# Optimization experiments

Measured on AMD Instinct MI355X. Metric: run time of the kernel, lower is better.

The kernel has to match this reference:

```python
import jax, jax.numpy as jnp
import numpy as np

B, S, C, MID = 32, 8192, 256, 128

def setup_inputs() -> dict:
    key = jax.random.key(0)
    k_x, k_w1, k_b1, k_w2, k_b2 = jax.random.split(key, 5)
    bound1 = 1.0 / np.sqrt(C)
    bound2 = 1.0 / np.sqrt(MID)
    return {
        "x": jax.random.normal(k_x, (B, S, C), dtype=jnp.float32),
        "W1": jax.random.uniform(k_w1, (C, MID), jnp.float32, -bound1, bound1),
        "b1": jax.random.uniform(k_b1, (MID,), jnp.float32, -bound1, bound1),
        "w2": jax.random.uniform(k_w2, (MID,), jnp.float32, -bound2, bound2),
        "b2": jax.random.uniform(k_b2, (), jnp.float32, -bound2, bound2),
    }

def reference(x, W1, b1, w2, b2):
    # scores: (B, S) — dropout is identity in eval mode
    h = jnp.tanh(jnp.einsum("bsc,cm->bsm", x, W1) + b1)       # (B, S, MID)
    scores = jnp.einsum("bsm,m->bs", h, w2) + b2              # (B, S)
    attn = jax.nn.softmax(scores, axis=-1)                    # softmax over seq
    out = jnp.einsum("bsc,bs->bc", x, attn)                   # weighted sum over seq
    return out
```

## Files before the change

### kernel.cpp

```cpp
#include <hip/hip_runtime.h>
#include <hip/hip_bf16.h>


typedef __attribute__((ext_vector_type(8))) short short8;
typedef __attribute__((ext_vector_type(4))) float f32x4;
typedef unsigned short u16;

constexpr int Bb = 32;
constexpr int Ss = 8192;
constexpr int Cc = 256;
constexpr int MIDm = 128;
constexpr int BM = 128;
constexpr int BK = 64;
constexpr int NCH = Cc / BK;
constexpr int NBLK = Bb * Ss / BM;
constexpr int BPB = Ss / BM;

__device__ __forceinline__ u16 f2bf(float f) {
  return __builtin_bit_cast(u16, __float2bfloat16(f));
}

__global__ __launch_bounds__(256) void wprep_kernel(
    const float* __restrict__ W1, u16* __restrict__ FB)
{
  const int t    = blockIdx.x * 256 + threadIdx.x;
  const int lane = t & 63;
  const int nt   = (t >> 6) & 3;
  const int kg   = (t >> 8) & 1;
  const int kc   = (t >> 9) & 3;
  const int wc   = (t >> 11) & 1;
  const int n    = wc * 64 + nt * 16 + (lane & 15);
  const int k0   = kc * 64 + kg * 32 + (lane >> 4) * 8;
  union { u16 v[8]; short8 s; } u;
  #pragma unroll
  for (int e = 0; e < 8; ++e) u.v[e] = f2bf(W1[(size_t)(k0 + e) * MIDm + n]);
  *(short8*)(FB + (size_t)t * 8) = u.s;
}

__global__ __launch_bounds__(256, 2) void fused_kernel(
    const float* __restrict__ x, const u16* __restrict__ FB,
    const float* __restrict__ b1, const float* __restrict__ w2,
    float* __restrict__ oPart, float* __restrict__ mPart, float* __restrict__ lPart)
{
  __shared__ __align__(16) float sX[2][BM * BK];
  __shared__ float sScore[2][BM];
  __shared__ float sP[BM];
  __shared__ float sMB, sLB;
  __shared__ __align__(16) float sO[4][Cc];

  const int tid  = threadIdx.x;
  const int lane = tid & 63;
  const int w    = tid >> 6;
  const int wr   = w >> 1;
  const int wc   = w & 1;
  const int q    = lane >> 4;
  const int ln   = lane & 15;
  const int row0 = blockIdx.x * BM;

  f32x4 acc[4][4];
  #pragma unroll
  for (int nt = 0; nt < 4; ++nt) {
    float bj = b1[64 * wc + 16 * nt + ln];
    #pragma unroll
    for (int mt = 0; mt < 4; ++mt) {
      acc[mt][nt][0] = bj; acc[mt][nt][1] = bj; acc[mt][nt][2] = bj; acc[mt][nt][3] = bj;
    }
  }

  const u16* fb = FB + ((size_t)wc * 2048 + lane) * 8;
  #define LDFRAG(kc, kg, nt) (*(const short8*)(fb + ((size_t)(kc)*512 + (kg)*256 + (nt)*64) * 8))

  #define STAGE(buf, kc)                                                              \
    {                                                                                 \
      _Pragma("unroll")                                                               \
      for (int r = 0; r < 8; ++r) {                                                   \
        int L    = r * 4096 + tid * 16;                                               \
        int row  = L >> 8;                                                            \
        int colb = (L & 255) ^ ((row & 7) << 4);                                      \
        const char* src = (const char*)x                                              \
            + ((size_t)(row0 + row) * Cc + (kc) * BK) * 4 + colb;                     \
        __builtin_amdgcn_global_load_lds(                                             \
            (const __attribute__((address_space(1))) void*)src,                       \
            (__attribute__((address_space(3))) void*)((char*)&sX[buf][0] + L),        \
            16, 0, 0);                                                                \
      }                                                                               \
    }

  short8 bfr[2][8];

  STAGE(0, 0);
  #pragma unroll
  for (int i = 0; i < 8; ++i) bfr[0][i] = LDFRAG(0, i >> 2, i & 3);
  __syncthreads();

  #pragma unroll
  for (int kc = 0; kc < NCH; ++kc) {
    const int cur = kc & 1;
    if (kc < NCH - 1) {
      STAGE(1 - cur, kc + 1);
      #pragma unroll
      for (int i = 0; i < 8; ++i) bfr[1 - cur][i] = LDFRAG(kc + 1, i >> 2, i & 3);
    }

    #pragma unroll
    for (int kg = 0; kg < 2; ++kg) {
      short8 af[4];
      #pragma unroll
      for (int mt = 0; mt < 4; ++mt) {
        const int row = 64 * wr + 16 * mt + ln;
        const int s   = (row & 7) << 4;
        const int c   = kg * 128 + q * 32;
        const char* base = (const char*)&sX[cur][0] + row * 256;
        float4 lo = *(const float4*)(base + ((c) ^ s));
        float4 hi = *(const float4*)(base + ((c + 16) ^ s));
        union { u16 v[8]; short8 s8; } t8;
        t8.v[0] = f2bf(lo.x); t8.v[1] = f2bf(lo.y); t8.v[2] = f2bf(lo.z); t8.v[3] = f2bf(lo.w);
        t8.v[4] = f2bf(hi.x); t8.v[5] = f2bf(hi.y); t8.v[6] = f2bf(hi.z); t8.v[7] = f2bf(hi.w);
        af[mt] = t8.s8;
      }
      #pragma unroll
      for (int nt = 0; nt < 4; ++nt)
        #pragma unroll
        for (int mt = 0; mt < 4; ++mt)
          acc[mt][nt] = __builtin_amdgcn_mfma_f32_16x16x32_bf16(
              af[mt], bfr[cur][kg * 4 + nt], acc[mt][nt], 0, 0, 0);
    }
    if (kc < NCH - 1) __syncthreads();
  }

  float w2v[4];
  #pragma unroll
  for (int nt = 0; nt < 4; ++nt) w2v[nt] = w2[64 * wc + 16 * nt + ln];

  float p[4][4];
  #pragma unroll
  for (int mt = 0; mt < 4; ++mt)
    #pragma unroll
    for (int r = 0; r < 4; ++r) p[mt][r] = 0.f;

  #pragma unroll
  for (int mt = 0; mt < 4; ++mt)
    #pragma unroll
    for (int nt = 0; nt < 4; ++nt)
      #pragma unroll
      for (int r = 0; r < 4; ++r)
        p[mt][r] += (1.0f - 2.0f / (__expf(2.0f * acc[mt][nt][r]) + 1.0f)) * w2v[nt];

  #pragma unroll
  for (int off = 1; off < 16; off <<= 1)
    #pragma unroll
    for (int mt = 0; mt < 4; ++mt)
      #pragma unroll
      for (int r = 0; r < 4; ++r)
        p[mt][r] += __shfl_xor(p[mt][r], off);

  __syncthreads();
  if (ln == 0) {
    #pragma unroll
    for (int mt = 0; mt < 4; ++mt)
      #pragma unroll
      for (int r = 0; r < 4; ++r)
        sScore[wc][64 * wr + 16 * mt + 4 * q + r] = p[mt][r];
  }
  __syncthreads();

  if (tid < BM) sP[tid] = sScore[0][tid] + sScore[1][tid];
  __syncthreads();
  if (w == 0) {
    float a = sP[lane], b = sP[lane + 64];
    float m = fmaxf(a, b);
    #pragma unroll
    for (int off = 1; off < 64; off <<= 1) m = fmaxf(m, __shfl_xor(m, off));
    float e0 = __expf(a - m), e1 = __expf(b - m);
    sP[lane] = e0; sP[lane + 64] = e1;
    float s = e0 + e1;
    #pragma unroll
    for (int off = 1; off < 64; off <<= 1) s += __shfl_xor(s, off);
    if (lane == 0) { sMB = m; sLB = s; }
  }
  __syncthreads();

  const int c4 = tid & 63;
  const int rg = tid >> 6;
  const float* xo = x + (size_t)(row0 + rg * 32) * Cc + c4 * 4;
  float4 o = make_float4(0.f, 0.f, 0.f, 0.f);
  #pragma unroll 8
  for (int r = 0; r < 32; ++r) {
    float pw = sP[rg * 32 + r];
    float4 xv = *(const float4*)(xo + (size_t)r * Cc);
    o.x = fmaf(pw, xv.x, o.x);
    o.y = fmaf(pw, xv.y, o.y);
    o.z = fmaf(pw, xv.z, o.z);
    o.w = fmaf(pw, xv.w, o.w);
  }
  *(float4*)&sO[rg][c4 * 4] = o;
  __syncthreads();

  float oc = sO[0][tid] + sO[1][tid] + sO[2][tid] + sO[3][tid];
  oPart[(size_t)blockIdx.x * Cc + tid] = oc;
  if (tid == 0) { mPart[blockIdx.x] = sMB; lPart[blockIdx.x] = sLB; }
}

__global__ __launch_bounds__(256) void combine_kernel(
    const float* __restrict__ oPart, const float* __restrict__ mPart,
    const float* __restrict__ lPart, float* __restrict__ out)
{
  const int b = blockIdx.x;
  const int t = threadIdx.x;
  float M = -3.4e38f;
  for (int k = 0; k < BPB; ++k) M = fmaxf(M, mPart[b * BPB + k]);
  float num = 0.f, den = 0.f;
  for (int k = 0; k < BPB; ++k) {
    float wgt = __expf(mPart[b * BPB + k] - M);
    den += wgt * lPart[b * BPB + k];
    num = fmaf(wgt, oPart[(size_t)(b * BPB + k) * Cc + t], num);
  }
  out[b * Cc + t] = num / den;
}

extern "C" void kernel_launch(void* const* d_in, const int* in_sizes, int n_in,
                              void* d_out, int out_size, void* d_ws, size_t ws_size,
                              hipStream_t stream)
{
  const float* x  = (const float*)d_in[0];
  const float* W1 = (const float*)d_in[1];
  const float* b1 = (const float*)d_in[2];
  const float* w2 = (const float*)d_in[3];
  float* out = (float*)d_out;

  u16*   FB    = (u16*)d_ws;
  float* oPart = (float*)((char*)d_ws + 65536);
  float* mPart = (float*)((char*)d_ws + 65536 + 2097152);
  float* lPart = (float*)((char*)d_ws + 65536 + 2097152 + 8192);

  wprep_kernel<<<16, 256, 0, stream>>>(W1, FB);
  fused_kernel<<<NBLK, 256, 0, stream>>>(x, FB, b1, w2, oPart, mPart, lPart);
  combine_kernel<<<Bb, Cc, 0, stream>>>(oPart, mPart, lPart, out);
}
```

Baseline: 97.35 us.

## Load x fragments directly from global into registers, drop LDS staging

Replaces the LDS double-buffered staging of x (global_load_lds with swizzle, plus block barriers) with per-thread direct global float4 loads into registers. These are prefetched two k-steps ahead, and the W1 fragment layout is re-indexed to 32-wide k chunks to match. This removes LDS traffic, the syncthreads per chunk and a big shared allocation, which may raise occupancy. In exchange, the two column-half waves both fetch the same x rows from global/L2, and register pressure goes up from holding the prefetched fragments.

```diff
diff --git a/kernel.cpp b/kernel.cpp
--- a/kernel.cpp
+++ b/kernel.cpp
@@ -11,8 +11,6 @@
 constexpr int Cc = 256;
 constexpr int MIDm = 128;
 constexpr int BM = 128;
-constexpr int BK = 64;
-constexpr int NCH = Cc / BK;
 constexpr int NBLK = Bb * Ss / BM;
 constexpr int BPB = Ss / BM;
 
@@ -26,11 +24,10 @@
   const int t    = blockIdx.x * 256 + threadIdx.x;
   const int lane = t & 63;
   const int nt   = (t >> 6) & 3;
-  const int kg   = (t >> 8) & 1;
-  const int kc   = (t >> 9) & 3;
+  const int kcc  = (t >> 8) & 7;
   const int wc   = (t >> 11) & 1;
   const int n    = wc * 64 + nt * 16 + (lane & 15);
-  const int k0   = kc * 64 + kg * 32 + (lane >> 4) * 8;
+  const int k0   = kcc * 32 + (lane >> 4) * 8;
   union { u16 v[8]; short8 s; } u;
   #pragma unroll
   for (int e = 0; e < 8; ++e) u.v[e] = f2bf(W1[(size_t)(k0 + e) * MIDm + n]);
@@ -42,7 +39,6 @@
     const float* __restrict__ b1, const float* __restrict__ w2,
     float* __restrict__ oPart, float* __restrict__ mPart, float* __restrict__ lPart)
 {
-  __shared__ __align__(16) float sX[2][BM * BK];
   __shared__ float sScore[2][BM];
   __shared__ float sP[BM];
   __shared__ float sMB, sLB;
@@ -57,6 +53,13 @@
   const int ln   = lane & 15;
   const int row0 = blockIdx.x * BM;
 
+  const float* pA[4];
+  #pragma unroll
+  for (int mt = 0; mt < 4; ++mt)
+    pA[mt] = x + (size_t)(row0 + 64 * wr + 16 * mt + ln) * Cc + q * 8;
+
+  const u16* fb = FB + ((size_t)wc * 2048 + lane) * 8;
+
   f32x4 acc[4][4];
   #pragma unroll
   for (int nt = 0; nt < 4; ++nt) {
@@ -67,65 +70,48 @@
     }
   }
 
-  const u16* fb = FB + ((size_t)wc * 2048 + lane) * 8;
-  #define LDFRAG(kc, kg, nt) (*(const short8*)(fb + ((size_t)(kc)*512 + (kg)*256 + (nt)*64) * 8))
-
-  #define STAGE(buf, kc)                                                              \
-    {                                                                                 \
-      _Pragma("unroll")                                                               \
-      for (int r = 0; r < 8; ++r) {                                                   \
-        int L    = r * 4096 + tid * 16;                                               \
-        int row  = L >> 8;                                                            \
-        int colb = (L & 255) ^ ((row & 7) << 4);                                      \
-        const char* src = (const char*)x                                              \
-            + ((size_t)(row0 + row) * Cc + (kc) * BK) * 4 + colb;                     \
-        __builtin_amdgcn_global_load_lds(                                             \
-            (const __attribute__((address_space(1))) void*)src,                       \
-            (__attribute__((address_space(3))) void*)((char*)&sX[buf][0] + L),        \
-            16, 0, 0);                                                                \
-      }                                                                               \
+  float4 A0[2][4], A1[2][4];
+  short8 Bf[2][4];
+
+  #define LOADA(ph, kk)                                                  \
+    { _Pragma("unroll")                                                  \
+      for (int mt = 0; mt < 4; ++mt) {                                   \
+        const float* p = pA[mt] + (kk) * 32;                             \
+        A0[ph][mt] = *(const float4*)p;                                  \
+        A1[ph][mt] = *(const float4*)(p + 4);                            \
+      } }
+  #define LOADB(ph, kk)                                                  \
+    { _Pragma("unroll")                                                  \
+      for (int nt = 0; nt < 4; ++nt)                                     \
+        Bf[ph][nt] = *(const short8*)(fb + ((size_t)(kk) * 256 + nt * 64) * 8); }
+
+  LOADA(0, 0) LOADB(0, 0)
+  LOADA(1, 1) LOADB(1, 1)
+
+  #pragma unroll
+  for (int kcc = 0; kcc < 8; ++kcc) {
+    const int ph = kcc & 1;
+
+    short8 af[4];
+    #pragma unroll
+    for (int mt = 0; mt < 4; ++mt) {
+      union { u16 v[8]; short8 s; } t8;
+      t8.v[0] = f2bf(A0[ph][mt].x); t8.v[1] = f2bf(A0[ph][mt].y);
+      t8.v[2] = f2bf(A0[ph][mt].z); t8.v[3] = f2bf(A0[ph][mt].w);
+      t8.v[4] = f2bf(A1[ph][mt].x); t8.v[5] = f2bf(A1[ph][mt].y);
+      t8.v[6] = f2bf(A1[ph][mt].z); t8.v[7] = f2bf(A1[ph][mt].w);
+      af[mt] = t8.s;
     }
-
-  short8 bfr[2][8];
-
-  STAGE(0, 0);
-  #pragma unroll
-  for (int i = 0; i < 8; ++i) bfr[0][i] = LDFRAG(0, i >> 2, i & 3);
-  __syncthreads();
-
-  #pragma unroll
-  for (int kc = 0; kc < NCH; ++kc) {
-    const int cur = kc & 1;
-    if (kc < NCH - 1) {
-      STAGE(1 - cur, kc + 1);
-      #pragma unroll
-      for (int i = 0; i < 8; ++i) bfr[1 - cur][i] = LDFRAG(kc + 1, i >> 2, i & 3);
-    }
-
-    #pragma unroll
-    for (int kg = 0; kg < 2; ++kg) {
-      short8 af[4];
-      #pragma unroll
-      for (int mt = 0; mt < 4; ++mt) {
-        const int row = 64 * wr + 16 * mt + ln;
-        const int s   = (row & 7) << 4;
-        const int c   = kg * 128 + q * 32;
-        const char* base = (const char*)&sX[cur][0] + row * 256;
-        float4 lo = *(const float4*)(base + ((c) ^ s));
-        float4 hi = *(const float4*)(base + ((c + 16) ^ s));
-        union { u16 v[8]; short8 s8; } t8;
-        t8.v[0] = f2bf(lo.x); t8.v[1] = f2bf(lo.y); t8.v[2] = f2bf(lo.z); t8.v[3] = f2bf(lo.w);
-        t8.v[4] = f2bf(hi.x); t8.v[5] = f2bf(hi.y); t8.v[6] = f2bf(hi.z); t8.v[7] = f2bf(hi.w);
-        af[mt] = t8.s8;
-      }
-      #pragma unroll
-      for (int nt = 0; nt < 4; ++nt)
-        #pragma unroll
-        for (int mt = 0; mt < 4; ++mt)
-          acc[mt][nt] = __builtin_amdgcn_mfma_f32_16x16x32_bf16(
-              af[mt], bfr[cur][kg * 4 + nt], acc[mt][nt], 0, 0, 0);
-    }
-    if (kc < NCH - 1) __syncthreads();
+    if (kcc < 6) LOADA(ph, kcc + 2)
+
+    #pragma unroll
+    for (int nt = 0; nt < 4; ++nt)
+      #pragma unroll
+      for (int mt = 0; mt < 4; ++mt)
+        acc[mt][nt] = __builtin_amdgcn_mfma_f32_16x16x32_bf16(
+            af[mt], Bf[ph][nt], acc[mt][nt], 0, 0, 0);
+
+    if (kcc < 6) LOADB(ph, kcc + 2)
   }
 
   float w2v[4];
@@ -154,7 +140,6 @@
       for (int r = 0; r < 4; ++r)
         p[mt][r] += __shfl_xor(p[mt][r], off);
 
-  __syncthreads();
   if (ln == 0) {
     #pragma unroll
     for (int mt = 0; mt < 4; ++mt)
```

Measured after the change: 129.0 us. 32.5% more time.

## Halve K-chunk to 32 and raise occupancy to four blocks per CU

Applied to the files above, without the earlier changes.

Reduces the staged x tile from 64 to 32 columns, so shared memory per block drops from about 64KB to about 32KB. The B-fragment register buffers are halved and launch bounds are raised to 4 blocks per CU to allow more resident waves to hide global-load latency. The weight-fragment layout in the prep kernel and the swizzled LDS staging are rewritten to match the 32-wide chunk. It also drops one barrier before the score write, and the chunk loop now has twice as many iterations and barriers.

```diff
diff --git a/kernel.cpp b/kernel.cpp
--- a/kernel.cpp
+++ b/kernel.cpp
@@ -11,7 +11,7 @@
 constexpr int Cc = 256;
 constexpr int MIDm = 128;
 constexpr int BM = 128;
-constexpr int BK = 64;
+constexpr int BK = 32;
 constexpr int NCH = Cc / BK;
 constexpr int NBLK = Bb * Ss / BM;
 constexpr int BPB = Ss / BM;
@@ -26,23 +26,22 @@
   const int t    = blockIdx.x * 256 + threadIdx.x;
   const int lane = t & 63;
   const int nt   = (t >> 6) & 3;
-  const int kg   = (t >> 8) & 1;
-  const int kc   = (t >> 9) & 3;
+  const int kcc  = (t >> 8) & 7;
   const int wc   = (t >> 11) & 1;
   const int n    = wc * 64 + nt * 16 + (lane & 15);
-  const int k0   = kc * 64 + kg * 32 + (lane >> 4) * 8;
+  const int k0   = kcc * 32 + (lane >> 4) * 8;
   union { u16 v[8]; short8 s; } u;
   #pragma unroll
   for (int e = 0; e < 8; ++e) u.v[e] = f2bf(W1[(size_t)(k0 + e) * MIDm + n]);
   *(short8*)(FB + (size_t)t * 8) = u.s;
 }
 
-__global__ __launch_bounds__(256, 2) void fused_kernel(
+__global__ __launch_bounds__(256, 4) void fused_kernel(
     const float* __restrict__ x, const u16* __restrict__ FB,
     const float* __restrict__ b1, const float* __restrict__ w2,
     float* __restrict__ oPart, float* __restrict__ mPart, float* __restrict__ lPart)
 {
-  __shared__ __align__(16) float sX[2][BM * BK];
+  __shared__ __align__(16) char sX[2][BM * BK * 4];
   __shared__ float sScore[2][BM];
   __shared__ float sP[BM];
   __shared__ float sMB, sLB;
@@ -68,29 +67,29 @@
   }
 
   const u16* fb = FB + ((size_t)wc * 2048 + lane) * 8;
-  #define LDFRAG(kc, kg, nt) (*(const short8*)(fb + ((size_t)(kc)*512 + (kg)*256 + (nt)*64) * 8))
+  #define LDFRAG(kcc, nt) (*(const short8*)(fb + ((size_t)(kcc) * 256 + (nt) * 64) * 8))
 
   #define STAGE(buf, kc)                                                              \
     {                                                                                 \
       _Pragma("unroll")                                                               \
-      for (int r = 0; r < 8; ++r) {                                                   \
-        int L    = r * 4096 + tid * 16;                                               \
-        int row  = L >> 8;                                                            \
-        int colb = (L & 255) ^ ((row & 7) << 4);                                      \
+      for (int r = 0; r < 4; ++r) {                                                   \
+        int L   = r * 4096 + tid * 16;                                                \
+        int row = L >> 7;                                                             \
+        int cb  = (L & 127) ^ ((row & 7) << 4);                                       \
         const char* src = (const char*)x                                              \
-            + ((size_t)(row0 + row) * Cc + (kc) * BK) * 4 + colb;                     \
+            + ((size_t)(row0 + row) * Cc + (size_t)(kc) * BK) * 4 + cb;               \
         __builtin_amdgcn_global_load_lds(                                             \
             (const __attribute__((address_space(1))) void*)src,                       \
-            (__attribute__((address_space(3))) void*)((char*)&sX[buf][0] + L),        \
+            (__attribute__((address_space(3))) void*)(&sX[buf][0] + L),               \
             16, 0, 0);                                                                \
       }                                                                               \
     }
 
-  short8 bfr[2][8];
+  short8 bfr[2][4];
 
   STAGE(0, 0);
   #pragma unroll
-  for (int i = 0; i < 8; ++i) bfr[0][i] = LDFRAG(0, i >> 2, i & 3);
+  for (int nt = 0; nt < 4; ++nt) bfr[0][nt] = LDFRAG(0, nt);
   __syncthreads();
 
   #pragma unroll
@@ -99,31 +98,23 @@
     if (kc < NCH - 1) {
       STAGE(1 - cur, kc + 1);
       #pragma unroll
-      for (int i = 0; i < 8; ++i) bfr[1 - cur][i] = LDFRAG(kc + 1, i >> 2, i & 3);
-    }
-
-    #pragma unroll
-    for (int kg = 0; kg < 2; ++kg) {
-      short8 af[4];
-      #pragma unroll
-      for (int mt = 0; mt < 4; ++mt) {
-        const int row = 64 * wr + 16 * mt + ln;
-        const int s   = (row & 7) << 4;
-        const int c   = kg * 128 + q * 32;
-        const char* base = (const char*)&sX[cur][0] + row * 256;
-        float4 lo = *(const float4*)(base + ((c) ^ s));
-        float4 hi = *(const float4*)(base + ((c + 16) ^ s));
-        union { u16 v[8]; short8 s8; } t8;
-        t8.v[0] = f2bf(lo.x); t8.v[1] = f2bf(lo.y); t8.v[2] = f2bf(lo.z); t8.v[3] = f2bf(lo.w);
-        t8.v[4] = f2bf(hi.x); t8.v[5] = f2bf(hi.y); t8.v[6] = f2bf(hi.z); t8.v[7] = f2bf(hi.w);
-        af[mt] = t8.s8;
-      }
+      for (int nt = 0; nt < 4; ++nt) bfr[1 - cur][nt] = LDFRAG(kc + 1, nt);
+    }
+
+    #pragma unroll
+    for (int mt = 0; mt < 4; ++mt) {
+      const int row = 64 * wr + 16 * mt + ln;
+      const int s   = (row & 7) << 4;
+      const char* base = &sX[cur][0] + row * 128;
+      float4 lo = *(const float4*)(base + ((q * 32) ^ s));
+      float4 hi = *(const float4*)(base + ((q * 32 + 16) ^ s));
+      union { u16 v[8]; short8 s8; } t8;
+      t8.v[0] = f2bf(lo.x); t8.v[1] = f2bf(lo.y); t8.v[2] = f2bf(lo.z); t8.v[3] = f2bf(lo.w);
+      t8.v[4] = f2bf(hi.x); t8.v[5] = f2bf(hi.y); t8.v[6] = f2bf(hi.z); t8.v[7] = f2bf(hi.w);
       #pragma unroll
       for (int nt = 0; nt < 4; ++nt)
-        #pragma unroll
-        for (int mt = 0; mt < 4; ++mt)
-          acc[mt][nt] = __builtin_amdgcn_mfma_f32_16x16x32_bf16(
-              af[mt], bfr[cur][kg * 4 + nt], acc[mt][nt], 0, 0, 0);
+        acc[mt][nt] = __builtin_amdgcn_mfma_f32_16x16x32_bf16(
+            t8.s8, bfr[cur][nt], acc[mt][nt], 0, 0, 0);
     }
     if (kc < NCH - 1) __syncthreads();
   }
@@ -154,7 +145,6 @@
       for (int r = 0; r < 4; ++r)
         p[mt][r] += __shfl_xor(p[mt][r], off);
 
-  __syncthreads();
   if (ln == 0) {
     #pragma unroll
     for (int mt = 0; mt < 4; ++mt)
```

After: 107.3 us. 10.2% more time.
